# Kernel optimization log

Measured on AMD Instinct MI355X. Metric: run time of the kernel, lower is better.

The kernel has to match this reference:

```python
import jax, jax.numpy as jnp
import numpy as np

N, IN_DIM, HID, OUT = 8192, 512, 256, 64
NEG_INF = -9e15


def setup_inputs() -> dict:
    key = jax.random.key(0)
    ks = jax.random.split(key, 7)
    X = jax.random.normal(ks[0], (N, IN_DIM), dtype=jnp.float32)
    A = jax.random.randint(ks[1], (N, N), 0, 2, dtype=jnp.int32)
    # fc1 (Linear): kaiming-uniform-ish init, exact dist irrelevant for correctness
    W1 = jax.random.normal(ks[2], (IN_DIM, HID), dtype=jnp.float32) / np.sqrt(IN_DIM)
    b1 = jnp.zeros((HID,), dtype=jnp.float32)
    # attention vector a: xavier_uniform(gain=1.414) on shape (2*HID, 1)
    lim = 1.414 * np.sqrt(6.0 / (2 * HID + 1))
    a = jax.random.uniform(ks[3], (2 * HID, 1), minval=-lim, maxval=lim, dtype=jnp.float32)
    Omega = jax.random.normal(ks[4], (HID, OUT), dtype=jnp.float32) * np.sqrt(2.0 / (HID + OUT))
    beta = jnp.zeros((OUT,), dtype=jnp.float32)
    return {"X": X, "A": A, "W1": W1, "b1": b1, "a": a, "Omega": Omega, "beta": beta}


def reference(X, A, W1, b1, a, Omega, beta):
    H1 = X @ W1 + b1                      # [N, HID]
    # score(i,j) = leakyrelu(a[:HID].H1_i + a[HID:].H1_j) -- computed via broadcast,
    # avoiding the O(N^2 * 2*HID) concat the torch code materializes.
    a1 = a[:HID, 0]                       # [HID]
    a2 = a[HID:, 0]                       # [HID]
    e = jax.nn.leaky_relu((H1 @ a1)[:, None] + (H1 @ a2)[None, :], negative_slope=0.2)  # [N, N]
    e = jnp.where(A > 0, e, NEG_INF)
    attention = jax.nn.softmax(e, axis=1)  # dropout_rate=0.0 -> identity
    H2 = attention @ H1                    # [N, HID]
    return jax.nn.sigmoid(H2 @ Omega + beta)  # [N, OUT]
```

## Files before the change

kernel.cpp:

```cpp
#include <hip/hip_runtime.h>
#include <hip/hip_bf16.h>


typedef float f32x4 __attribute__((ext_vector_type(4)));
typedef short s16x8 __attribute__((ext_vector_type(8)));

#define NN 8192
#define INDIM 512
#define HIDD 256
#define OUTD 64

static __device__ __forceinline__ short f2bf(float x) {
    __hip_bfloat16 h = __float2bfloat16(x);
    return __builtin_bit_cast(short, h);
}

static __device__ __forceinline__ void split_bf(float x, short& hi, short& lo) {
    short h = f2bf(x);
    unsigned int hb = ((unsigned int)(unsigned short)h) << 16;
    float hf = __builtin_bit_cast(float, hb);
    hi = h;
    lo = f2bf(x - hf);
}

__global__ void __launch_bounds__(256)
k_packA(const int* __restrict__ A, unsigned int* __restrict__ Apk) {
    const int i = blockIdx.x;
    const int t = threadIdx.x;
    const int ks = t >> 6, q = (t >> 4) & 3, kk0 = t & 15;
    const int* Ar = A + (size_t)i * NN;
    unsigned int out = 0;
#pragma unroll
    for (int kkq = 0; kkq < 4; ++kkq) {
        const int kk = kk0 * 4 + kkq;
        const int c0 = ks * 2048 + kk * 32 + q * 8;
        int4 v0 = *(const int4*)(Ar + c0);
        int4 v1 = *(const int4*)(Ar + c0 + 4);
        unsigned int b = 0;
        b |= (v0.x > 0) ? 1u : 0u;
        b |= (v0.y > 0) ? 2u : 0u;
        b |= (v0.z > 0) ? 4u : 0u;
        b |= (v0.w > 0) ? 8u : 0u;
        b |= (v1.x > 0) ? 16u : 0u;
        b |= (v1.y > 0) ? 32u : 0u;
        b |= (v1.z > 0) ? 64u : 0u;
        b |= (v1.w > 0) ? 128u : 0u;
        out |= b << (kkq * 8);
    }
    Apk[(size_t)i * 256 + t] = out;
}

__global__ void k_splitW1(const float* __restrict__ W1,
                          short* __restrict__ W1Thi, short* __restrict__ W1Tlo) {
    int t = blockIdx.x * 256 + threadIdx.x;
    int n = t >> 9;
    int k = t & 511;
    float x = W1[k * 256 + n];
    short hi, lo; split_bf(x, hi, lo);
    W1Thi[t] = hi;
    W1Tlo[t] = lo;
}

__global__ void __launch_bounds__(256, 2)
k_h1(const float* __restrict__ X, const short* __restrict__ W1Thi,
     const short* __restrict__ W1Tlo, const float* __restrict__ b1,
     const float* __restrict__ avec, unsigned short* __restrict__ H1TB,
     float* __restrict__ alw, float* __restrict__ bew, float* __restrict__ uvw) {
    __shared__ float s1p[4][16];
    __shared__ float s2p[4][16];
    const int tid = threadIdx.x;
    const int wn = tid >> 6, lane = tid & 63;
    const int q = lane >> 4, m16 = lane & 15;
    const int i0 = blockIdx.x * 16;
    const int irow = i0 + m16;

    f32x4 zero4 = {0.f, 0.f, 0.f, 0.f};
    f32x4 acc[4];
#pragma unroll
    for (int nt = 0; nt < 4; ++nt) acc[nt] = zero4;

    const float* Xrow = X + (size_t)irow * INDIM;
    for (int kk = 0; kk < INDIM; kk += 32) {
        const int k0 = kk + q * 8;
        float4 xa = *(const float4*)(Xrow + k0);
        float4 xb = *(const float4*)(Xrow + k0 + 4);
        float xs[8] = {xa.x, xa.y, xa.z, xa.w, xb.x, xb.y, xb.z, xb.w};
        s16x8 ahi, alo;
#pragma unroll
        for (int j = 0; j < 8; ++j) { short h, l; split_bf(xs[j], h, l); ahi[j] = h; alo[j] = l; }
#pragma unroll
        for (int nt = 0; nt < 4; ++nt) {
            const int n = wn * 64 + nt * 16 + m16;
            s16x8 bhi = *(const s16x8*)(W1Thi + n * INDIM + k0);
            s16x8 blo = *(const s16x8*)(W1Tlo + n * INDIM + k0);
            acc[nt] = __builtin_amdgcn_mfma_f32_16x16x32_bf16(ahi, bhi, acc[nt], 0, 0, 0);
            acc[nt] = __builtin_amdgcn_mfma_f32_16x16x32_bf16(ahi, blo, acc[nt], 0, 0, 0);
            acc[nt] = __builtin_amdgcn_mfma_f32_16x16x32_bf16(alo, bhi, acc[nt], 0, 0, 0);
        }
    }

    float p1[4] = {0.f, 0.f, 0.f, 0.f};
    float p2[4] = {0.f, 0.f, 0.f, 0.f};
    const int rowbase = i0 + q * 4;
    const int chunk = rowbase >> 5, win = rowbase & 31;
#pragma unroll
    for (int nt = 0; nt < 4; ++nt) {
        const int col = wn * 64 + nt * 16 + m16;
        const float b1v = b1[col];
        const float a1v = avec[col];
        const float a2v = avec[HIDD + col];
        float v0 = acc[nt][0] + b1v;
        float v1 = acc[nt][1] + b1v;
        float v2 = acc[nt][2] + b1v;
        float v3 = acc[nt][3] + b1v;
        ushort4 us;
        us.x = (unsigned short)f2bf(v0);
        us.y = (unsigned short)f2bf(v1);
        us.z = (unsigned short)f2bf(v2);
        us.w = (unsigned short)f2bf(v3);
        *(ushort4*)(H1TB + (size_t)chunk * 8192 + col * 32 + win) = us;
        p1[0] += v0 * a1v; p1[1] += v1 * a1v; p1[2] += v2 * a1v; p1[3] += v3 * a1v;
        p2[0] += v0 * a2v; p2[1] += v1 * a2v; p2[2] += v2 * a2v; p2[3] += v3 * a2v;
    }
#pragma unroll
    for (int off = 1; off < 16; off <<= 1) {
#pragma unroll
        for (int r = 0; r < 4; ++r) {
            p1[r] += __shfl_xor(p1[r], off);
            p2[r] += __shfl_xor(p2[r], off);
        }
    }
    if (m16 == 0) {
#pragma unroll
        for (int r = 0; r < 4; ++r) {
            s1p[wn][q * 4 + r] = p1[r];
            s2p[wn][q * 4 + r] = p2[r];
        }
    }
    __syncthreads();
    if (tid < 16) {
        const int i = i0 + tid;
        float s1 = s1p[0][tid] + s1p[1][tid] + s1p[2][tid] + s1p[3][tid];
        float s2 = s2p[0][tid] + s2p[1][tid] + s2p[2][tid] + s2p[3][tid];
        alw[i] = expf(s1);
        bew[i] = expf(0.2f * s1);
        uvw[2 * i]     = expf(s2);
        uvw[2 * i + 1] = expf(0.2f * s2);
    }
}

__global__ void __launch_bounds__(256, 4)
k_attn(const unsigned int* __restrict__ Apk, const unsigned short* __restrict__ H1TB,
       const float* __restrict__ alw, const float* __restrict__ bew,
       const float* __restrict__ uvw,
       float* __restrict__ H2acc, float* __restrict__ Zw) {
    __shared__ unsigned short tile[2][8192];

    const int tid = threadIdx.x;
    const int wave = tid >> 6, lane = tid & 63;
    const int q = lane >> 4, m16 = lane & 15;
    const int wm = wave & 1, wn = wave >> 1;
    const int mb = blockIdx.x & 255;
    const int ks = blockIdx.x >> 8;
    const int i = mb * 32 + wm * 16 + m16;
    const float al = alw[i], be = bew[i];

    const unsigned short* gp = H1TB + (size_t)ks * 64 * 8192 + tid * 8;
    __attribute__((address_space(3))) unsigned short* tl =
        (__attribute__((address_space(3))) unsigned short*)&tile[0][0];

    const unsigned int* Ab = Apk + (size_t)i * 256 + ks * 64 + q * 16;
    const float* uvp = uvw + 2 * (ks * 2048 + q * 8);

    f32x4 zero4 = {0.f, 0.f, 0.f, 0.f};
    f32x4 acc[8];
#pragma unroll
    for (int nt = 0; nt < 8; ++nt) acc[nt] = zero4;
    float zacc = 0.f;

#pragma unroll
    for (int c = 0; c < 4; ++c)
        __builtin_amdgcn_global_load_lds(
            (const __attribute__((address_space(1))) void*)(gp + c * 2048),
            (__attribute__((address_space(3))) void*)(tl + c * 2048 + tid * 8),
            16, 0, 0);
    gp += 8192;

    float4 uv0 = *(const float4*)(uvp);
    float4 uv1 = *(const float4*)(uvp + 4);
    float4 uv2 = *(const float4*)(uvp + 8);
    float4 uv3 = *(const float4*)(uvp + 12);
    uvp += 64;
    unsigned int a4 = Ab[0];

    for (int kk4 = 0; kk4 < 16; ++kk4) {
        unsigned int a4n = Ab[(kk4 + 1) & 15];
#pragma unroll
        for (int kkq = 0; kkq < 4; ++kkq) {
            const int kk = kk4 * 4 + kkq;
            const unsigned int ab = a4 >> (kkq * 8);

            float wv[8];
            wv[0] = (ab & 1u)   ? fmaxf(al * uv0.x, be * uv0.y) : 0.f;
            wv[1] = (ab & 2u)   ? fmaxf(al * uv0.z, be * uv0.w) : 0.f;
            wv[2] = (ab & 4u)   ? fmaxf(al * uv1.x, be * uv1.y) : 0.f;
            wv[3] = (ab & 8u)   ? fmaxf(al * uv1.z, be * uv1.w) : 0.f;
            wv[4] = (ab & 16u)  ? fmaxf(al * uv2.x, be * uv2.y) : 0.f;
            wv[5] = (ab & 32u)  ? fmaxf(al * uv2.z, be * uv2.w) : 0.f;
            wv[6] = (ab & 64u)  ? fmaxf(al * uv3.x, be * uv3.y) : 0.f;
            wv[7] = (ab & 128u) ? fmaxf(al * uv3.z, be * uv3.w) : 0.f;
            zacc += (wv[0] + wv[1] + wv[2] + wv[3]) + (wv[4] + wv[5] + wv[6] + wv[7]);
            s16x8 af;
#pragma unroll
            for (int j = 0; j < 8; ++j) af[j] = f2bf(wv[j]);

            __builtin_amdgcn_sched_barrier(0);
            if (kkq == 0) asm volatile("s_waitcnt vmcnt(1)" ::: "memory");
            else          asm volatile("s_waitcnt vmcnt(0)" ::: "memory");
            __builtin_amdgcn_s_barrier();
            __builtin_amdgcn_sched_barrier(0);

            if (kk < 63) {
                uv0 = *(const float4*)(uvp);
                uv1 = *(const float4*)(uvp + 4);
                uv2 = *(const float4*)(uvp + 8);
                uv3 = *(const float4*)(uvp + 12);
                uvp += 64;
                const int nb = ((kk + 1) & 1) * 8192;
#pragma unroll
                for (int c = 0; c < 4; ++c)
                    __builtin_amdgcn_global_load_lds(
                        (const __attribute__((address_space(1))) void*)(gp + c * 2048),
                        (__attribute__((address_space(3))) void*)(tl + nb + c * 2048 + tid * 8),
                        16, 0, 0);
                gp += 8192;
            }

            const unsigned short* tb = &tile[kk & 1][0];
#pragma unroll
            for (int nt = 0; nt < 8; ++nt) {
                s16x8 bfv = *(const s16x8*)(tb + (wn * 128 + nt * 16 + m16) * 32 + q * 8);
                acc[nt] = __builtin_amdgcn_mfma_f32_16x16x32_bf16(af, bfv, acc[nt], 0, 0, 0);
            }
        }
        a4 = a4n;
    }

    zacc += __shfl_xor(zacc, 16);
    zacc += __shfl_xor(zacc, 32);
    if (wn == 0 && q == 0) atomicAdd(&Zw[i], zacc);

    const int rowbase = mb * 32 + wm * 16 + q * 4;
#pragma unroll
    for (int nt = 0; nt < 8; ++nt) {
        const int col = wn * 128 + nt * 16 + m16;
#pragma unroll
        for (int r = 0; r < 4; ++r)
            atomicAdd(&H2acc[(size_t)(rowbase + r) * HIDD + col], acc[nt][r]);
    }
}

__global__ void __launch_bounds__(256)
k_out(const float* __restrict__ H2acc, const float* __restrict__ Zw,
      const float* __restrict__ Omega, const float* __restrict__ beta,
      float* __restrict__ out) {
    __shared__ float om[HIDD * OUTD];
    const int tid = threadIdx.x;
    for (int idx = tid; idx < HIDD * OUTD; idx += 256) om[idx] = Omega[idx];
    __syncthreads();
    const int wave = tid >> 6, o = tid & 63;
    const float bv = beta[o];
    for (int rr = 0; rr < 8; ++rr) {
        const int i = blockIdx.x * 32 + wave * 8 + rr;
        const float4* H2v = (const float4*)(H2acc + (size_t)i * HIDD);
        float acc = 0.f;
#pragma unroll 4
        for (int c4 = 0; c4 < 64; ++c4) {
            float4 h = H2v[c4];
            const int cb = c4 * 4;
            acc = fmaf(h.x, om[(cb + 0) * OUTD + o], acc);
            acc = fmaf(h.y, om[(cb + 1) * OUTD + o], acc);
            acc = fmaf(h.z, om[(cb + 2) * OUTD + o], acc);
            acc = fmaf(h.w, om[(cb + 3) * OUTD + o], acc);
        }
        const float zinv = 1.0f / Zw[i];
        const float logit = acc * zinv + bv;
        out[(size_t)i * OUTD + o] = 1.0f / (1.0f + expf(-logit));
    }
}

extern "C" void kernel_launch(void* const* d_in, const int* in_sizes, int n_in,
                              void* d_out, int out_size, void* d_ws, size_t ws_size,
                              hipStream_t stream) {
    const float* X     = (const float*)d_in[0];
    const int*   A     = (const int*)d_in[1];
    const float* W1    = (const float*)d_in[2];
    const float* b1    = (const float*)d_in[3];
    const float* avec  = (const float*)d_in[4];
    const float* Omega = (const float*)d_in[5];
    const float* beta  = (const float*)d_in[6];
    float* out = (float*)d_out;

    char* ws = (char*)d_ws;
    unsigned short* H1TB = (unsigned short*)(ws + 0);
    short* W1Thi = (short*)(ws + 4194304);
    short* W1Tlo = (short*)(ws + 4456448);
    float* alw   = (float*)(ws + 4718592);
    float* bew   = (float*)(ws + 4751360);
    float* uvw   = (float*)(ws + 4784128);
    float* Zw    = (float*)(ws + 4849664);
    float* H2acc = (float*)(ws + 4882432);
    unsigned int* Apk = (unsigned int*)(ws + 13271040);

    hipMemsetAsync(Zw, 0, 32768 + 8388608, stream);

    k_packA<<<8192, 256, 0, stream>>>(A, Apk);
    k_splitW1<<<512, 256, 0, stream>>>(W1, W1Thi, W1Tlo);
    k_h1<<<512, 256, 0, stream>>>(X, W1Thi, W1Tlo, b1, avec, H1TB, alw, bew, uvw);
    k_attn<<<1024, 256, 0, stream>>>(Apk, H1TB, alw, bew, uvw, H2acc, Zw);
    k_out<<<256, 256, 0, stream>>>(H2acc, Zw, Omega, beta, out);
}
```

Measured before the change: 544.7 us.

## Drop LDS staging in attention kernel and replace atomics with split-K partial buffers

The attention kernel no longer stages H1 tiles through LDS with double buffering and barriers. Each wave now loads its B fragments directly from global memory, and blocks shrink to 16 rows with 4 waves splitting the 256 columns. Split-K partial results are written to separate per-slice buffers instead of atomically added, and the output kernel sums the four slices; this also removes the memset. The smaller blocks, raised occupancy bound, and lack of sync are meant to improve latency hiding, but they lose the LDS reuse of H1 across row groups and add larger partial buffers.

```diff
diff --git a/kernel.cpp b/kernel.cpp
--- a/kernel.cpp
+++ b/kernel.cpp
@@ -149,57 +149,49 @@
     }
 }
 
-__global__ void __launch_bounds__(256, 4)
+__global__ void __launch_bounds__(256, 8)
 k_attn(const unsigned int* __restrict__ Apk, const unsigned short* __restrict__ H1TB,
        const float* __restrict__ alw, const float* __restrict__ bew,
        const float* __restrict__ uvw,
-       float* __restrict__ H2acc, float* __restrict__ Zw) {
-    __shared__ unsigned short tile[2][8192];
-
+       float* __restrict__ H2s, float* __restrict__ Zs) {
     const int tid = threadIdx.x;
-    const int wave = tid >> 6, lane = tid & 63;
+    const int wn = tid >> 6, lane = tid & 63;
     const int q = lane >> 4, m16 = lane & 15;
-    const int wm = wave & 1, wn = wave >> 1;
-    const int mb = blockIdx.x & 255;
-    const int ks = blockIdx.x >> 8;
-    const int i = mb * 32 + wm * 16 + m16;
+    const int ks = blockIdx.x & 3;
+    const int mb = blockIdx.x >> 2;
+    const int i = mb * 16 + m16;
     const float al = alw[i], be = bew[i];
 
-    const unsigned short* gp = H1TB + (size_t)ks * 64 * 8192 + tid * 8;
-    __attribute__((address_space(3))) unsigned short* tl =
-        (__attribute__((address_space(3))) unsigned short*)&tile[0][0];
-
+    const unsigned short* hbase =
+        H1TB + (size_t)ks * 64 * 8192 + (wn * 64 + m16) * 32 + q * 8;
     const unsigned int* Ab = Apk + (size_t)i * 256 + ks * 64 + q * 16;
-    const float* uvp = uvw + 2 * (ks * 2048 + q * 8);
+    const float* uvb = uvw + 2 * (ks * 2048 + q * 8);
 
     f32x4 zero4 = {0.f, 0.f, 0.f, 0.f};
-    f32x4 acc[8];
-#pragma unroll
-    for (int nt = 0; nt < 8; ++nt) acc[nt] = zero4;
+    f32x4 acc[4];
+#pragma unroll
+    for (int nt = 0; nt < 4; ++nt) acc[nt] = zero4;
     float zacc = 0.f;
 
-#pragma unroll
-    for (int c = 0; c < 4; ++c)
-        __builtin_amdgcn_global_load_lds(
-            (const __attribute__((address_space(1))) void*)(gp + c * 2048),
-            (__attribute__((address_space(3))) void*)(tl + c * 2048 + tid * 8),
-            16, 0, 0);
-    gp += 8192;
-
-    float4 uv0 = *(const float4*)(uvp);
-    float4 uv1 = *(const float4*)(uvp + 4);
-    float4 uv2 = *(const float4*)(uvp + 8);
-    float4 uv3 = *(const float4*)(uvp + 12);
-    uvp += 64;
     unsigned int a4 = Ab[0];
 
     for (int kk4 = 0; kk4 < 16; ++kk4) {
-        unsigned int a4n = Ab[(kk4 + 1) & 15];
+        const unsigned int a4n = Ab[(kk4 + 1) & 15];
 #pragma unroll
         for (int kkq = 0; kkq < 4; ++kkq) {
             const int kk = kk4 * 4 + kkq;
+            const float* uvp = uvb + kk * 64;
+            float4 uv0 = *(const float4*)(uvp);
+            float4 uv1 = *(const float4*)(uvp + 4);
+            float4 uv2 = *(const float4*)(uvp + 8);
+            float4 uv3 = *(const float4*)(uvp + 12);
+            const unsigned short* hq = hbase + (size_t)kk * 8192;
+            s16x8 b0 = *(const s16x8*)(hq);
+            s16x8 b1 = *(const s16x8*)(hq + 512);
+            s16x8 b2 = *(const s16x8*)(hq + 1024);
+            s16x8 b3 = *(const s16x8*)(hq + 1536);
+
             const unsigned int ab = a4 >> (kkq * 8);
-
             float wv[8];
             wv[0] = (ab & 1u)   ? fmaxf(al * uv0.x, be * uv0.y) : 0.f;
             wv[1] = (ab & 2u)   ? fmaxf(al * uv0.z, be * uv0.w) : 0.f;
@@ -214,54 +206,30 @@
 #pragma unroll
             for (int j = 0; j < 8; ++j) af[j] = f2bf(wv[j]);
 
-            __builtin_amdgcn_sched_barrier(0);
-            if (kkq == 0) asm volatile("s_waitcnt vmcnt(1)" ::: "memory");
-            else          asm volatile("s_waitcnt vmcnt(0)" ::: "memory");
-            __builtin_amdgcn_s_barrier();
-            __builtin_amdgcn_sched_barrier(0);
-
-            if (kk < 63) {
-                uv0 = *(const float4*)(uvp);
-                uv1 = *(const float4*)(uvp + 4);
-                uv2 = *(const float4*)(uvp + 8);
-                uv3 = *(const float4*)(uvp + 12);
-                uvp += 64;
-                const int nb = ((kk + 1) & 1) * 8192;
-#pragma unroll
-                for (int c = 0; c < 4; ++c)
-                    __builtin_amdgcn_global_load_lds(
-                        (const __attribute__((address_space(1))) void*)(gp + c * 2048),
-                        (__attribute__((address_space(3))) void*)(tl + nb + c * 2048 + tid * 8),
-                        16, 0, 0);
-                gp += 8192;
-            }
-
-            const unsigned short* tb = &tile[kk & 1][0];
-#pragma unroll
-            for (int nt = 0; nt < 8; ++nt) {
-                s16x8 bfv = *(const s16x8*)(tb + (wn * 128 + nt * 16 + m16) * 32 + q * 8);
-                acc[nt] = __builtin_amdgcn_mfma_f32_16x16x32_bf16(af, bfv, acc[nt], 0, 0, 0);
-            }
+            acc[0] = __builtin_amdgcn_mfma_f32_16x16x32_bf16(af, b0, acc[0], 0, 0, 0);
+            acc[1] = __builtin_amdgcn_mfma_f32_16x16x32_bf16(af, b1, acc[1], 0, 0, 0);
+            acc[2] = __builtin_amdgcn_mfma_f32_16x16x32_bf16(af, b2, acc[2], 0, 0, 0);
+            acc[3] = __builtin_amdgcn_mfma_f32_16x16x32_bf16(af, b3, acc[3], 0, 0, 0);
         }
         a4 = a4n;
     }
 
     zacc += __shfl_xor(zacc, 16);
     zacc += __shfl_xor(zacc, 32);
-    if (wn == 0 && q == 0) atomicAdd(&Zw[i], zacc);
-
-    const int rowbase = mb * 32 + wm * 16 + q * 4;
-#pragma unroll
-    for (int nt = 0; nt < 8; ++nt) {
-        const int col = wn * 128 + nt * 16 + m16;
+    if (wn == 0 && q == 0) Zs[(size_t)ks * NN + i] = zacc;
+
+    float* Hb = H2s + ((size_t)ks * NN + (size_t)mb * 16) * HIDD;
+#pragma unroll
+    for (int nt = 0; nt < 4; ++nt) {
+        const int col = wn * 64 + nt * 16 + m16;
 #pragma unroll
         for (int r = 0; r < 4; ++r)
-            atomicAdd(&H2acc[(size_t)(rowbase + r) * HIDD + col], acc[nt][r]);
+            Hb[(size_t)(q * 4 + r) * HIDD + col] = acc[nt][r];
     }
 }
 
 __global__ void __launch_bounds__(256)
-k_out(const float* __restrict__ H2acc, const float* __restrict__ Zw,
+k_out(const float* __restrict__ H2s, const float* __restrict__ Zs,
       const float* __restrict__ Omega, const float* __restrict__ beta,
       float* __restrict__ out) {
     __shared__ float om[HIDD * OUTD];
@@ -272,19 +240,26 @@
     const float bv = beta[o];
     for (int rr = 0; rr < 8; ++rr) {
         const int i = blockIdx.x * 32 + wave * 8 + rr;
-        const float4* H2v = (const float4*)(H2acc + (size_t)i * HIDD);
+        const float4* h0 = (const float4*)(H2s + (size_t)i * HIDD);
+        const float4* h1 = (const float4*)(H2s + (size_t)(NN + i) * HIDD);
+        const float4* h2 = (const float4*)(H2s + (size_t)(2 * NN + i) * HIDD);
+        const float4* h3 = (const float4*)(H2s + (size_t)(3 * NN + i) * HIDD);
         float acc = 0.f;
 #pragma unroll 4
         for (int c4 = 0; c4 < 64; ++c4) {
-            float4 h = H2v[c4];
+            float4 a = h0[c4], b = h1[c4], c = h2[c4], d = h3[c4];
+            const float sx = (a.x + b.x) + (c.x + d.x);
+            const float sy = (a.y + b.y) + (c.y + d.y);
+            const float sz = (a.z + b.z) + (c.z + d.z);
+            const float sw = (a.w + b.w) + (c.w + d.w);
             const int cb = c4 * 4;
-            acc = fmaf(h.x, om[(cb + 0) * OUTD + o], acc);
-            acc = fmaf(h.y, om[(cb + 1) * OUTD + o], acc);
-            acc = fmaf(h.z, om[(cb + 2) * OUTD + o], acc);
-            acc = fmaf(h.w, om[(cb + 3) * OUTD + o], acc);
-        }
-        const float zinv = 1.0f / Zw[i];
-        const float logit = acc * zinv + bv;
+            acc = fmaf(sx, om[(cb + 0) * OUTD + o], acc);
+            acc = fmaf(sy, om[(cb + 1) * OUTD + o], acc);
+            acc = fmaf(sz, om[(cb + 2) * OUTD + o], acc);
+            acc = fmaf(sw, om[(cb + 3) * OUTD + o], acc);
+        }
+        const float z = (Zs[i] + Zs[NN + i]) + (Zs[2 * NN + i] + Zs[3 * NN + i]);
+        const float logit = acc / z + bv;
         out[(size_t)i * OUTD + o] = 1.0f / (1.0f + expf(-logit));
     }
 }
@@ -308,15 +283,14 @@
     float* alw   = (float*)(ws + 4718592);
     float* bew   = (float*)(ws + 4751360);
     float* uvw   = (float*)(ws + 4784128);
-    float* Zw    = (float*)(ws + 4849664);
-    float* H2acc = (float*)(ws + 4882432);
-    unsigned int* Apk = (unsigned int*)(ws + 13271040);
-
-    hipMemsetAsync(Zw, 0, 32768 + 8388608, stream);
+    unsigned int* Apk = (unsigned int*)(ws + 4849664);
+    float* H2s   = (float*)(ws + 13238272);
+    float* Zs    = (float*)(ws + 46792704);
+
 
     k_packA<<<8192, 256, 0, stream>>>(A, Apk);
     k_splitW1<<<512, 256, 0, stream>>>(W1, W1Thi, W1Tlo);
     k_h1<<<512, 256, 0, stream>>>(X, W1Thi, W1Tlo, b1, avec, H1TB, alw, bew, uvw);
-    k_attn<<<1024, 256, 0, stream>>>(Apk, H1TB, alw, bew, uvw, H2acc, Zw);
-    k_out<<<256, 256, 0, stream>>>(H2acc, Zw, Omega, beta, out);
-}
+    k_attn<<<2048, 256, 0, stream>>>(Apk, H1TB, alw, bew, uvw, H2s, Zs);
+    k_out<<<256, 256, 0, stream>>>(H2s, Zs, Omega, beta, out);
+}
```

Result: slower. 745.1 us (+36.8%).
